# Kernel tuning notes

Hardware: AMD Instinct MI355X
Metric: run time of the kernel (lower is better)

## Reference

```python
import jax, jax.numpy as jnp
import numpy as np

D_MODEL = 1024
N_HEADS = 16
D_HEAD = D_MODEL // N_HEADS
B, T = 4, 2048


def setup_inputs() -> dict:
    key = jax.random.key(0)
    k1, k2, k3 = jax.random.split(key, 3)
    x = jax.random.normal(k1, (B, T, D_MODEL), dtype=jnp.float32)
    # causal mask, broadcastable [1,1,T,T]; 0 => masked
    mask = jnp.tril(jnp.ones((T, T), dtype=jnp.int32))[None, None, :, :]
    # torch Linear weight is [out,in]; store transposed for x @ W
    Wqkv = jax.random.normal(k2, (D_MODEL, 3 * D_MODEL), dtype=jnp.float32) * (D_MODEL ** -0.5)
    Wout = jax.random.normal(k3, (D_MODEL, D_MODEL), dtype=jnp.float32) * (D_MODEL ** -0.5)
    return {"x": x, "mask": mask, "Wqkv": Wqkv, "Wout": Wout}


def reference(x, mask, Wqkv, Wout):
    Bb, Tt, C = x.shape
    qkv = (x @ Wqkv).reshape(Bb, Tt, 3, N_HEADS, D_HEAD)
    qkv = jnp.transpose(qkv, (2, 0, 3, 1, 4))  # [3,B,H,T,Dh]
    q, k, v = qkv[0], qkv[1], qkv[2]
    scale = 1.0 / jnp.sqrt(jnp.asarray(D_HEAD, x.dtype))
    att = jnp.einsum("bhqd,bhkd->bhqk", q, k) * scale  # [B,H,T,T]
    att = jnp.where(mask[:, :, :Tt, :Tt] == 0, jnp.asarray(-jnp.inf, att.dtype), att)
    att = jax.nn.softmax(att, axis=-1)
    out = jnp.einsum("bhqk,bhkd->bhqd", att, v)  # [B,H,T,Dh]
    out = jnp.transpose(out, (0, 2, 1, 3)).reshape(Bb, Tt, C)
    return out @ Wout
```

## Files before the change

kernel.cpp:

```cpp
#include <hip/hip_runtime.h>
#include <hip/hip_bf16.h>

#define BATCH   4
#define SEQ     2048
#define DMODEL  1024
#define NHEADS  16
#define DHEAD   64
#define BT      (BATCH*SEQ)

typedef unsigned short u16;
typedef unsigned int u32;
typedef __bf16 bf16x8 __attribute__((ext_vector_type(8)));
typedef float  f32x4  __attribute__((ext_vector_type(4)));
typedef float  f32x16 __attribute__((ext_vector_type(16)));
typedef u16    u16x8  __attribute__((ext_vector_type(8)));
typedef u16    u16x4  __attribute__((ext_vector_type(4)));
typedef u32    u32x4  __attribute__((ext_vector_type(4)));

#define MFMA16(a,b,c) __builtin_amdgcn_mfma_f32_16x16x32_bf16((a),(b),(c),0,0,0)
#define MFMA32(a,b,c) __builtin_amdgcn_mfma_f32_32x32x16_bf16((a),(b),(c),0,0,0)

__device__ __forceinline__ u16 f2b(float f) {
  return __builtin_bit_cast(u16, (__bf16)f);
}
__device__ __forceinline__ u32 pack2(float lo, float hi) {
  return (u32)f2b(lo) | ((u32)f2b(hi) << 16);
}

__device__ __forceinline__ void gload_lds16(const u16* g, u16* l) {
  __builtin_amdgcn_global_load_lds(
      (const __attribute__((address_space(1))) void*)g,
      (__attribute__((address_space(3))) void*)l, 16, 0, 0);
}

__global__ __launch_bounds__(256) void cvt_bf16_kernel(
    const float* __restrict__ in, u16* __restrict__ out, int n8) {
  int i = blockIdx.x * 256 + threadIdx.x;
  if (i >= n8) return;
  const float4* p = (const float4*)(in + (long)i * 8);
  float4 a = p[0], b = p[1];
  u16x8 o;
  o[0]=f2b(a.x); o[1]=f2b(a.y); o[2]=f2b(a.z); o[3]=f2b(a.w);
  o[4]=f2b(b.x); o[5]=f2b(b.y); o[6]=f2b(b.z); o[7]=f2b(b.w);
  *(u16x8*)(out + (long)i * 8) = o;
}

__global__ __launch_bounds__(256) void transpose_cvt_kernel(
    const float* __restrict__ W, u16* __restrict__ Wt, int K, int N) {
  __shared__ float tile[32][33];
  int tx = threadIdx.x & 31, ty = threadIdx.x >> 5;
  int bx = blockIdx.x, by = blockIdx.y;
  #pragma unroll
  for (int r = 0; r < 32; r += 8)
    tile[ty + r][tx] = W[(long)(by * 32 + ty + r) * N + bx * 32 + tx];
  __syncthreads();
  #pragma unroll
  for (int r = 0; r < 32; r += 8)
    Wt[(long)(bx * 32 + ty + r) * K + by * 32 + tx] = f2b(tile[tx][ty + r]);
}

template<int MODE>
__global__ __launch_bounds__(256) void gemm_bt_kernel(
    const u16* __restrict__ A, const u16* __restrict__ Bt,
    float* __restrict__ C,
    u16* __restrict__ Qb, u16* __restrict__ Kb, u16* __restrict__ Vt,
    int M, int N, int K) {
  __shared__ u16 lA[2][128 * 64];
  __shared__ u16 lB[2][128 * 64];
  const int tid = threadIdx.x;
  const int l = tid & 63, w = tid >> 6;
  const int g = l >> 4, c16 = l & 15;
  const int bn = blockIdx.x, bm = blockIdx.y;
  const int wm = w >> 1, wn = w & 1;
  const int srow = tid >> 3;
  const int sslot = tid & 7;
  const int scol = ((sslot ^ (srow & 7)) << 3);
  const u16* Ab = A  + (long)(bm * 128 + srow) * K + scol;
  const u16* Bb = Bt + (long)(bn * 128 + srow) * K + scol;
  const int ldst = srow * 64 + sslot * 8;

  f32x4 acc[4][4];
  #pragma unroll
  for (int i = 0; i < 4; ++i)
    #pragma unroll
    for (int j = 0; j < 4; ++j)
      #pragma unroll
      for (int e = 0; e < 4; ++e) acc[i][j][e] = 0.f;

  const int nt = K >> 6;
  #pragma unroll
  for (int h = 0; h < 4; ++h) {
    gload_lds16(Ab + (long)h * 32 * K, &lA[0][h * 32 * 64 + ldst]);
    gload_lds16(Bb + (long)h * 32 * K, &lB[0][h * 32 * 64 + ldst]);
  }
  asm volatile("s_waitcnt vmcnt(0)" ::: "memory");
  __builtin_amdgcn_s_barrier();

  #pragma unroll 1
  for (int t = 0; t < nt; ++t) {
    const int cur = t & 1;
    if (t + 1 < nt) {
      const long koff = (long)(t + 1) * 64;
      #pragma unroll
      for (int h = 0; h < 4; ++h) {
        gload_lds16(Ab + (long)h * 32 * K + koff, &lA[cur ^ 1][h * 32 * 64 + ldst]);
        gload_lds16(Bb + (long)h * 32 * K + koff, &lB[cur ^ 1][h * 32 * 64 + ldst]);
      }
      asm volatile("s_waitcnt vmcnt(8)" ::: "memory");
    } else {
      asm volatile("s_waitcnt vmcnt(0)" ::: "memory");
    }
    __builtin_amdgcn_s_barrier();
    asm volatile("" ::: "memory");

    const char* a0 = (const char*)&lA[cur][0];
    const char* b0 = (const char*)&lB[cur][0];
    const int swz = (c16 & 7) << 4;
    __builtin_amdgcn_s_setprio(1);
    #pragma unroll
    for (int ks = 0; ks < 2; ++ks) {
      bf16x8 af[4], bfr[4];
      #pragma unroll
      for (int mf = 0; mf < 4; ++mf)
        af[mf] = *(const bf16x8*)(a0 + (wm * 64 + mf * 16 + c16) * 128 +
                                  (((ks * 4 + g) * 16) ^ swz));
      #pragma unroll
      for (int nf = 0; nf < 4; ++nf)
        bfr[nf] = *(const bf16x8*)(b0 + (wn * 64 + nf * 16 + c16) * 128 +
                                   (((ks * 4 + g) * 16) ^ swz));
      #pragma unroll
      for (int nf = 0; nf < 4; ++nf)
        #pragma unroll
        for (int mf = 0; mf < 4; ++mf)
          acc[mf][nf] = MFMA16(af[mf], bfr[nf], acc[mf][nf]);
    }
    __builtin_amdgcn_s_setprio(0);
    asm volatile("" ::: "memory");
    __builtin_amdgcn_s_barrier();
  }

  #pragma unroll
  for (int mf = 0; mf < 4; ++mf) {
    const int trow_base = bm * 128 + wm * 64 + mf * 16 + g * 4;
    #pragma unroll
    for (int nf = 0; nf < 4; ++nf) {
      const int col = bn * 128 + wn * 64 + nf * 16 + c16;
      #pragma unroll
      for (int r = 0; r < 4; ++r) {
        const float v = acc[mf][nf][r];
        const int trow = trow_base + r;
        if constexpr (MODE == 0) {
          C[(long)trow * N + col] = v;
        } else {
          const int s = col >> 10;
          const int rem = col & 1023;
          const int h = rem >> 6, d = rem & 63;
          const int b = trow >> 11, tt = trow & 2047;
          const int bh = b * NHEADS + h;
          if (s == 0)      Qb[((long)bh * SEQ + tt) * DHEAD + d] = f2b(v * 0.125f);
          else if (s == 1) Kb[((long)bh * SEQ + tt) * DHEAD + d] = f2b(v);
          else             Vt[((long)bh * DHEAD + d) * SEQ + tt] = f2b(v);
        }
      }
    }
  }
}

__global__ __launch_bounds__(512, 2) void attn_kernel(
    const u16* __restrict__ Qb, const u16* __restrict__ Kb,
    const u16* __restrict__ Vt, u16* __restrict__ Ob) {
  __shared__ u16 kbuf[2][64 * 64];
  __shared__ u16 vbuf[2][64 * 64];
  const int tid = threadIdx.x;
  const int lane = tid & 63, w = tid >> 6;
  const int c = lane & 31, g2 = lane >> 5;
  const int bh = blockIdx.x;
  const int b = bh >> 4, h = bh & 15;
  const u16* Kbh = Kb + (long)bh * SEQ * DHEAD;
  const u16* Vbh = Vt + (long)bh * DHEAD * SEQ;

  const int srow = lane >> 3;
  const int sswz = ((lane & 7) * 16) ^ (srow << 4);
  const int swz  = (c & 7) << 4;

  #pragma unroll 1
  for (int pass = 0; pass < 2; ++pass) {
    const int qblk = pass ? (7 - (int)blockIdx.y) : (int)blockIdx.y;
    const int qb0 = qblk * 256;
    const int qrow0 = qb0 + w * 32;
    const int nt = qb0 / 64 + 4;
    const int mytiles = (qrow0 + 31) / 64 + 1;

    bf16x8 qf[4];
    {
      const u16* Qrow = Qb + ((long)bh * SEQ + qrow0 + c) * DHEAD + g2 * 8;
      #pragma unroll
      for (int ds = 0; ds < 4; ++ds)
        qf[ds] = *(const bf16x8*)(Qrow + ds * 16);
    }

    f32x16 o0, o1;
    #pragma unroll
    for (int e = 0; e < 16; ++e) { o0[e] = 0.f; o1[e] = 0.f; }
    float m_run = -__builtin_inff(), l_run = 0.f;

    {
      const u16* gk = Kbh + (long)(w * 8 + srow) * DHEAD + (sswz >> 1);
      gload_lds16(gk, &kbuf[0][w * 512]);
      const u16* gv = Vbh + (long)(w * 8 + srow) * SEQ + (sswz >> 1);
      gload_lds16(gv, &vbuf[0][w * 512]);
    }
    asm volatile("s_waitcnt vmcnt(0)" ::: "memory");
    __builtin_amdgcn_s_barrier();

    #pragma unroll 1
    for (int t = 0; t < nt; ++t) {
      const int kv = t * 64;
      const int cur = t & 1;
      if (t + 1 < nt) {
        const int kv2 = kv + 64;
        const u16* gk = Kbh + (long)(kv2 + w * 8 + srow) * DHEAD + (sswz >> 1);
        gload_lds16(gk, &kbuf[cur ^ 1][w * 512]);
        const u16* gv = Vbh + (long)(w * 8 + srow) * SEQ + kv2 + (sswz >> 1);
        gload_lds16(gv, &vbuf[cur ^ 1][w * 512]);
        asm volatile("s_waitcnt vmcnt(2)" ::: "memory");
      } else {
        asm volatile("s_waitcnt vmcnt(0)" ::: "memory");
      }
      __builtin_amdgcn_s_barrier();

      if (t < mytiles) {
        f32x16 p0, p1;
        #pragma unroll
        for (int e = 0; e < 16; ++e) { p0[e] = 0.f; p1[e] = 0.f; }
        const char* kb = (const char*)&kbuf[cur][0];
        __builtin_amdgcn_s_setprio(1);
        #pragma unroll
        for (int ds = 0; ds < 4; ++ds) {
          bf16x8 aK0 = *(const bf16x8*)(kb + c * 128 + ((ds * 32 + g2 * 16) ^ swz));
          bf16x8 aK1 = *(const bf16x8*)(kb + (32 + c) * 128 + ((ds * 32 + g2 * 16) ^ swz));
          p0 = MFMA32(aK0, qf[ds], p0);
          p1 = MFMA32(aK1, qf[ds], p1);
        }
        __builtin_amdgcn_s_setprio(0);

        if (kv + 63 > qrow0) {
          const int q = qrow0 + c;
          #pragma unroll
          for (int r = 0; r < 16; ++r) {
            const int koff = (r & 3) + 8 * (r >> 2) + 4 * g2;
            if (kv + koff > q)      p0[r] = -__builtin_inff();
            if (kv + 32 + koff > q) p1[r] = -__builtin_inff();
          }
        }

        float vmax = p0[0];
        #pragma unroll
        for (int e = 1; e < 16; ++e) vmax = fmaxf(vmax, p0[e]);
        #pragma unroll
        for (int e = 0; e < 16; ++e) vmax = fmaxf(vmax, p1[e]);
        vmax = fmaxf(vmax, __shfl_xor(vmax, 32, 64));
        const float mnew = fmaxf(m_run, vmax);
        const float scale = __builtin_amdgcn_exp2f((m_run - mnew) * 1.44269504f);
        m_run = mnew;
        float ps = 0.f;
        #pragma unroll
        for (int e = 0; e < 16; ++e) {
          p0[e] = __builtin_amdgcn_exp2f((p0[e] - mnew) * 1.44269504f);
          p1[e] = __builtin_amdgcn_exp2f((p1[e] - mnew) * 1.44269504f);
          ps += p0[e] + p1[e];
        }
        ps += __shfl_xor(ps, 32, 64);
        l_run = l_run * scale + ps;
        #pragma unroll
        for (int e = 0; e < 16; ++e) { o0[e] *= scale; o1[e] *= scale; }

        u32x4 pbw[4];
        #pragma unroll
        for (int s = 0; s < 4; ++s) {
          const int base = 8 * (s & 1);
          float e0, e1, e2, e3, e4, e5, e6, e7;
          if (s < 2) {
            e0=p0[base+0]; e1=p0[base+1]; e2=p0[base+2]; e3=p0[base+3];
            e4=p0[base+4]; e5=p0[base+5]; e6=p0[base+6]; e7=p0[base+7];
          } else {
            e0=p1[base+0]; e1=p1[base+1]; e2=p1[base+2]; e3=p1[base+3];
            e4=p1[base+4]; e5=p1[base+5]; e6=p1[base+6]; e7=p1[base+7];
          }
          const u32 w01 = pack2(e0, e1), w23 = pack2(e2, e3);
          const u32 w45 = pack2(e4, e5), w67 = pack2(e6, e7);
          const u32 sendA = g2 ? w01 : w45;
          const u32 sendB = g2 ? w23 : w67;
          const u32 recvA = (u32)__shfl_xor((int)sendA, 32, 64);
          const u32 recvB = (u32)__shfl_xor((int)sendB, 32, 64);
          pbw[s][0] = g2 ? recvA : w01;
          pbw[s][1] = g2 ? recvB : w23;
          pbw[s][2] = g2 ? w45 : recvA;
          pbw[s][3] = g2 ? w67 : recvB;
        }

        const char* vb = (const char*)&vbuf[cur][0];
        __builtin_amdgcn_s_setprio(1);
        #pragma unroll
        for (int s = 0; s < 4; ++s) {
          const bf16x8 pv = __builtin_bit_cast(bf16x8, pbw[s]);
          bf16x8 aV0 = *(const bf16x8*)(vb + c * 128 + ((s * 32 + g2 * 16) ^ swz));
          bf16x8 aV1 = *(const bf16x8*)(vb + (32 + c) * 128 + ((s * 32 + g2 * 16) ^ swz));
          o0 = MFMA32(aV0, pv, o0);
          o1 = MFMA32(aV1, pv, o1);
        }
        __builtin_amdgcn_s_setprio(0);
      }
      asm volatile("" ::: "memory");
      __builtin_amdgcn_s_barrier();
    }

    const float rinv = 1.f / l_run;
    const int q = qrow0 + c;
    u16* orow = Ob + ((long)b * SEQ + q) * DMODEL + h * DHEAD;
    #pragma unroll
    for (int m = 0; m < 4; ++m) {
      u16x4 v0, v1;
      #pragma unroll
      for (int e = 0; e < 4; ++e) {
        v0[e] = f2b(o0[4 * m + e] * rinv);
        v1[e] = f2b(o1[4 * m + e] * rinv);
      }
      const int d0 = 8 * m + 4 * g2;
      *(u16x4*)(orow + d0) = v0;
      *(u16x4*)(orow + 32 + d0) = v1;
    }
  }
}

extern "C" void kernel_launch(void* const* d_in, const int* in_sizes, int n_in,
                              void* d_out, int out_size, void* d_ws, size_t ws_size,
                              hipStream_t stream) {
  const float* x    = (const float*)d_in[0];
  const float* Wqkv = (const float*)d_in[2];
  const float* Wout = (const float*)d_in[3];
  float* out = (float*)d_out;
  char* ws = (char*)d_ws;
  u16* Xb  = (u16*)(ws + 0);
  u16* Wt1 = (u16*)(ws + 16777216);
  u16* Wt2 = (u16*)(ws + 23068672);
  u16* Qb  = (u16*)(ws + 25165824);
  u16* Kb  = (u16*)(ws + 41943040);
  u16* Vt  = (u16*)(ws + 58720256);
  u16* Ob  = (u16*)(ws + 75497472);

  cvt_bf16_kernel<<<4096, 256, 0, stream>>>(x, Xb, BT * DMODEL / 8);
  transpose_cvt_kernel<<<dim3(96, 32), 256, 0, stream>>>(Wqkv, Wt1, DMODEL, 3 * DMODEL);
  transpose_cvt_kernel<<<dim3(32, 32), 256, 0, stream>>>(Wout, Wt2, DMODEL, DMODEL);
  gemm_bt_kernel<1><<<dim3(24, 64), 256, 0, stream>>>(
      Xb, Wt1, nullptr, Qb, Kb, Vt, BT, 3 * DMODEL, DMODEL);
  attn_kernel<<<dim3(64, 4), 512, 0, stream>>>(Qb, Kb, Vt, Ob);
  gemm_bt_kernel<0><<<dim3(8, 64), 256, 0, stream>>>(
      Ob, Wt2, out, nullptr, nullptr, nullptr, BT, DMODEL, DMODEL);
}
```

Before: 296.8 us.

## Restructure GEMM to 512-thread 32x32 MFMA with B operand loaded directly to registers

The projection GEMM now uses 8 waves and 32x32x16 MFMA instead of 16x16x32. Only A is staged through LDS. The B fragments are read straight from global memory into registers each k-step, which removes the B LDS buffer and its ds_reads. The QKV GEMM uses a 128x256 tile (NBF=2), while the output GEMM keeps 128x128. This aims to cut LDS traffic and raise MFMA efficiency, but B loads are now uncached global reads on the critical path, with hand-tuned vmcnt counts that must match exactly.

```diff
diff --git a/kernel.cpp b/kernel.cpp
--- a/kernel.cpp
+++ b/kernel.cpp
@@ -17,7 +17,6 @@
 typedef u16    u16x4  __attribute__((ext_vector_type(4)));
 typedef u32    u32x4  __attribute__((ext_vector_type(4)));
 
-#define MFMA16(a,b,c) __builtin_amdgcn_mfma_f32_16x16x32_bf16((a),(b),(c),0,0,0)
 #define MFMA32(a,b,c) __builtin_amdgcn_mfma_f32_32x32x16_bf16((a),(b),(c),0,0,0)
 
 __device__ __forceinline__ u16 f2b(float f) {
@@ -59,80 +58,75 @@
     Wt[(long)(bx * 32 + ty + r) * K + by * 32 + tx] = f2b(tile[tx][ty + r]);
 }
 
-template<int MODE>
-__global__ __launch_bounds__(256) void gemm_bt_kernel(
+template<int MODE, int NBF>
+__global__ __launch_bounds__(512, 2) void gemm_bt_kernel(
     const u16* __restrict__ A, const u16* __restrict__ Bt,
     float* __restrict__ C,
     u16* __restrict__ Qb, u16* __restrict__ Kb, u16* __restrict__ Vt,
     int M, int N, int K) {
   __shared__ u16 lA[2][128 * 64];
-  __shared__ u16 lB[2][128 * 64];
   const int tid = threadIdx.x;
-  const int l = tid & 63, w = tid >> 6;
-  const int g = l >> 4, c16 = l & 15;
+  const int lane = tid & 63, w = tid >> 6;
+  const int c = lane & 31, g2 = lane >> 5;
+  const int wm = w >> 2, wn = w & 3;
   const int bn = blockIdx.x, bm = blockIdx.y;
-  const int wm = w >> 1, wn = w & 1;
-  const int srow = tid >> 3;
-  const int sslot = tid & 7;
-  const int scol = ((sslot ^ (srow & 7)) << 3);
-  const u16* Ab = A  + (long)(bm * 128 + srow) * K + scol;
-  const u16* Bb = Bt + (long)(bn * 128 + srow) * K + scol;
-  const int ldst = srow * 64 + sslot * 8;
-
-  f32x4 acc[4][4];
+  const int srow8 = tid >> 3, sslot = tid & 7;
+  const int scol = (sslot ^ (srow8 & 7)) << 3;
+  const u16* Ab = A + (long)(bm * 128 + srow8) * K + scol;
+  const int ldst = srow8 * 64 + sslot * 8;
+  const int bcol = bn * (NBF * 128) + wn * (NBF * 32) + c;
+  const u16* Bb = Bt + (long)bcol * K + g2 * 8;
+
+  f32x16 acc[2][NBF];
   #pragma unroll
-  for (int i = 0; i < 4; ++i)
-    #pragma unroll
-    for (int j = 0; j < 4; ++j)
-      #pragma unroll
-      for (int e = 0; e < 4; ++e) acc[i][j][e] = 0.f;
+  for (int mf = 0; mf < 2; ++mf)
+    #pragma unroll
+    for (int nf = 0; nf < NBF; ++nf)
+      #pragma unroll
+      for (int e = 0; e < 16; ++e) acc[mf][nf][e] = 0.f;
 
   const int nt = K >> 6;
-  #pragma unroll
-  for (int h = 0; h < 4; ++h) {
-    gload_lds16(Ab + (long)h * 32 * K, &lA[0][h * 32 * 64 + ldst]);
-    gload_lds16(Bb + (long)h * 32 * K, &lB[0][h * 32 * 64 + ldst]);
-  }
+  gload_lds16(Ab, &lA[0][ldst]);
+  gload_lds16(Ab + (long)64 * K, &lA[0][64 * 64 + ldst]);
   asm volatile("s_waitcnt vmcnt(0)" ::: "memory");
   __builtin_amdgcn_s_barrier();
 
   #pragma unroll 1
   for (int t = 0; t < nt; ++t) {
     const int cur = t & 1;
+    bf16x8 bfrag[NBF][4];
+    #pragma unroll
+    for (int nf = 0; nf < NBF; ++nf)
+      #pragma unroll
+      for (int ks = 0; ks < 4; ++ks)
+        bfrag[nf][ks] = *(const bf16x8*)(Bb + (long)nf * 32 * K + t * 64 + ks * 16);
     if (t + 1 < nt) {
-      const long koff = (long)(t + 1) * 64;
-      #pragma unroll
-      for (int h = 0; h < 4; ++h) {
-        gload_lds16(Ab + (long)h * 32 * K + koff, &lA[cur ^ 1][h * 32 * 64 + ldst]);
-        gload_lds16(Bb + (long)h * 32 * K + koff, &lB[cur ^ 1][h * 32 * 64 + ldst]);
-      }
-      asm volatile("s_waitcnt vmcnt(8)" ::: "memory");
+      const long ko = (long)(t + 1) * 64;
+      gload_lds16(Ab + ko, &lA[cur ^ 1][ldst]);
+      gload_lds16(Ab + (long)64 * K + ko, &lA[cur ^ 1][64 * 64 + ldst]);
+      if constexpr (NBF == 2) asm volatile("s_waitcnt vmcnt(10)" ::: "memory");
+      else                    asm volatile("s_waitcnt vmcnt(6)" ::: "memory");
     } else {
-      asm volatile("s_waitcnt vmcnt(0)" ::: "memory");
+      if constexpr (NBF == 2) asm volatile("s_waitcnt vmcnt(8)" ::: "memory");
+      else                    asm volatile("s_waitcnt vmcnt(4)" ::: "memory");
     }
     __builtin_amdgcn_s_barrier();
-    asm volatile("" ::: "memory");
 
     const char* a0 = (const char*)&lA[cur][0];
-    const char* b0 = (const char*)&lB[cur][0];
-    const int swz = (c16 & 7) << 4;
+    const int swz = (c & 7) << 4;
     __builtin_amdgcn_s_setprio(1);
     #pragma unroll
-    for (int ks = 0; ks < 2; ++ks) {
-      bf16x8 af[4], bfr[4];
-      #pragma unroll
-      for (int mf = 0; mf < 4; ++mf)
-        af[mf] = *(const bf16x8*)(a0 + (wm * 64 + mf * 16 + c16) * 128 +
-                                  (((ks * 4 + g) * 16) ^ swz));
-      #pragma unroll
-      for (int nf = 0; nf < 4; ++nf)
-        bfr[nf] = *(const bf16x8*)(b0 + (wn * 64 + nf * 16 + c16) * 128 +
-                                   (((ks * 4 + g) * 16) ^ swz));
-      #pragma unroll
-      for (int nf = 0; nf < 4; ++nf)
-        #pragma unroll
-        for (int mf = 0; mf < 4; ++mf)
-          acc[mf][nf] = MFMA16(af[mf], bfr[nf], acc[mf][nf]);
+    for (int ks = 0; ks < 4; ++ks) {
+      bf16x8 af[2];
+      #pragma unroll
+      for (int mf = 0; mf < 2; ++mf)
+        af[mf] = *(const bf16x8*)(a0 + (wm * 64 + mf * 32 + c) * 128 +
+                                  ((ks * 32 + g2 * 16) ^ swz));
+      #pragma unroll
+      for (int mf = 0; mf < 2; ++mf)
+        #pragma unroll
+        for (int nf = 0; nf < NBF; ++nf)
+          acc[mf][nf] = MFMA32(af[mf], bfrag[nf][ks], acc[mf][nf]);
     }
     __builtin_amdgcn_s_setprio(0);
     asm volatile("" ::: "memory");
@@ -140,15 +134,14 @@
   }
 
   #pragma unroll
-  for (int mf = 0; mf < 4; ++mf) {
-    const int trow_base = bm * 128 + wm * 64 + mf * 16 + g * 4;
-    #pragma unroll
-    for (int nf = 0; nf < 4; ++nf) {
-      const int col = bn * 128 + wn * 64 + nf * 16 + c16;
-      #pragma unroll
-      for (int r = 0; r < 4; ++r) {
+  for (int mf = 0; mf < 2; ++mf) {
+    #pragma unroll
+    for (int nf = 0; nf < NBF; ++nf) {
+      const int col = bn * (NBF * 128) + wn * (NBF * 32) + nf * 32 + c;
+      #pragma unroll
+      for (int r = 0; r < 16; ++r) {
+        const int trow = bm * 128 + wm * 64 + mf * 32 + (r & 3) + 8 * (r >> 2) + 4 * g2;
         const float v = acc[mf][nf][r];
-        const int trow = trow_base + r;
         if constexpr (MODE == 0) {
           C[(long)trow * N + col] = v;
         } else {
@@ -352,9 +345,9 @@
   cvt_bf16_kernel<<<4096, 256, 0, stream>>>(x, Xb, BT * DMODEL / 8);
   transpose_cvt_kernel<<<dim3(96, 32), 256, 0, stream>>>(Wqkv, Wt1, DMODEL, 3 * DMODEL);
   transpose_cvt_kernel<<<dim3(32, 32), 256, 0, stream>>>(Wout, Wt2, DMODEL, DMODEL);
-  gemm_bt_kernel<1><<<dim3(24, 64), 256, 0, stream>>>(
+  gemm_bt_kernel<1, 2><<<dim3(12, 64), 512, 0, stream>>>(
       Xb, Wt1, nullptr, Qb, Kb, Vt, BT, 3 * DMODEL, DMODEL);
   attn_kernel<<<dim3(64, 4), 512, 0, stream>>>(Qb, Kb, Vt, Ob);
-  gemm_bt_kernel<0><<<dim3(8, 64), 256, 0, stream>>>(
+  gemm_bt_kernel<0, 1><<<dim3(8, 64), 512, 0, stream>>>(
       Ob, Wt2, out, nullptr, nullptr, nullptr, BT, DMODEL, DMODEL);
 }
```

Result: slower. 358.9 us (+20.9%).
